# Optimization experiments

Measured on AMD Instinct MI355X. Metric: run time of the kernel, lower is better.

The kernel has to match this reference:

```python
import jax, jax.numpy as jnp
import numpy as np

B, S, D, H = 4, 2048, 512, 8
HD = D // H  # head width = 64

def setup_inputs() -> dict:
    key = jax.random.key(0)
    ks = jax.random.split(key, 7)
    x = jax.random.normal(ks[0], (B, S, D), dtype=jnp.float32)
    mask = jnp.ones((B, S), dtype=jnp.int32)
    # torch nn.Linear(dim, dim): weight [out, in], bias [out]
    sc = 1.0 / np.sqrt(D)
    Wq = jax.random.uniform(ks[1], (D, D), jnp.float32, -sc, sc)
    bq = jax.random.uniform(ks[2], (D,), jnp.float32, -sc, sc)
    Wk = jax.random.uniform(ks[3], (D, D), jnp.float32, -sc, sc)
    bk = jax.random.uniform(ks[4], (D,), jnp.float32, -sc, sc)
    Wv = jax.random.uniform(ks[5], (D, D), jnp.float32, -sc, sc)
    bv = jax.random.uniform(ks[6], (D,), jnp.float32, -sc, sc)
    return {"x": x, "mask": mask, "Wq": Wq, "bq": bq, "Wk": Wk, "bk": bk, "Wv": Wv, "bv": bv}

def reference(x, mask, Wq, bq, Wk, bk, Wv, bv):
    # QKV projections (torch Linear: x @ W.T + b)
    q = jnp.einsum('bsd,ed->bse', x, Wq) + bq
    k = jnp.einsum('bsd,ed->bse', x, Wk) + bk
    v = jnp.einsum('bsd,ed->bse', x, Wv) + bv
    # split heads -> (B, H, S, HD)
    q = q.reshape(B, S, H, HD).transpose(0, 2, 1, 3)
    k = k.reshape(B, S, H, HD).transpose(0, 2, 1, 3)
    v = v.reshape(B, S, H, HD).transpose(0, 2, 1, 3)
    scores = jnp.einsum('bhqd,bhkd->bhqk', q, k) / np.sqrt(HD).astype(np.float32)
    m = mask[:, None, None, :].astype(scores.dtype)  # (B,1,1,S)
    scores = scores - 10000.0 * (1.0 - m)
    attn = jax.nn.softmax(scores, axis=-1)  # dropout is identity in eval mode
    h = jnp.einsum('bhqk,bhkd->bhqd', attn, v)
    h = h.transpose(0, 2, 1, 3).reshape(B, S, D)
    return h
```

## Files before the change

### kernel.cpp

```cpp
#include <hip/hip_runtime.h>
#include <hip/hip_bf16.h>

#define Bb 4
#define Ss 2048
#define Dd 512
#define Hh 8
#define HD 64
#define NX (Bb*Ss*Dd)
#define NW (3*Dd*Dd)

typedef __attribute__((ext_vector_type(8))) short bf8_t;
typedef __attribute__((ext_vector_type(4))) float f4_t;
typedef unsigned int u32;
typedef __attribute__((ext_vector_type(4))) unsigned int u32x4;

typedef const unsigned int __attribute__((address_space(1)))* gas_t;
typedef unsigned int __attribute__((address_space(3)))* las_t;

#define LOG2E 1.44269504088896f
#define MBIAS_C (-10000.0f * LOG2E)

template<bool V> struct BoolC { static constexpr bool value = V; };

__device__ __forceinline__ short cvt1(float f) {
  __hip_bfloat16 h = __float2bfloat16(f);
  union { __hip_bfloat16 hh; short ss; } u; u.hh = h; return u.ss;
}

__device__ __forceinline__ u32 pkrn(float a, float b) {
  union { __hip_bfloat162 h2; u32 u; } v;
  v.h2 = __float22bfloat162_rn(make_float2(a, b));
  return v.u;
}

__device__ __forceinline__ bf8_t pack8(float4 f0, float4 f1) {
  union { bf8_t v8; u32x4 u4; } u;
  u.u4.x = pkrn(f0.x, f0.y); u.u4.y = pkrn(f0.z, f0.w);
  u.u4.z = pkrn(f1.x, f1.y); u.u4.w = pkrn(f1.z, f1.w);
  return u.v8;
}

__device__ __forceinline__ void gload_lds16(const void* g, void* l) {
  __builtin_amdgcn_global_load_lds((gas_t)g, (las_t)l, 16, 0, 0);
}

__global__ __launch_bounds__(256) void convert_kernel(
    const float* __restrict__ x, const float* __restrict__ Wq,
    const float* __restrict__ Wk, const float* __restrict__ Wv,
    short* __restrict__ xb, short* __restrict__ Wb)
{
  size_t i = ((size_t)blockIdx.x * 256 + threadIdx.x) * 8;
  const float* src; short* dst;
  if (i < (size_t)NX) { src = x + i; dst = xb + i; }
  else {
    size_t j = i - NX;
    int ws = (int)(j >> 18);
    const float* W = (ws == 0) ? Wq : (ws == 1) ? Wk : Wv;
    src = W + (j & 0x3FFFF); dst = Wb + j;
  }
  float4 f0 = *(const float4*)src;
  float4 f1 = *(const float4*)(src + 4);
  *(bf8_t*)dst = pack8(f0, f1);
}

__global__ __launch_bounds__(256, 2) void qkv_proj_kernel(
    const short* __restrict__ xb, const short* __restrict__ Wb,
    const float* __restrict__ bq, const float* __restrict__ bk,
    const float* __restrict__ bv,
    short* __restrict__ Qg, short* __restrict__ Kg, short* __restrict__ Vtg)
{
  __shared__ short SM[32768];
  short* As0 = SM;
  short* Bs0 = SM + 16384;
  const int p = blockIdx.y >> 2;
  const short* __restrict__ W = Wb + (size_t)p * Dd * Dd;
  const float* __restrict__ bias = (p==0) ? bq : (p==1) ? bk : bv;
  const int m0 = blockIdx.x * 128;
  const int n0 = (blockIdx.y & 3) * 128;
  const int tid = threadIdx.x;
  const int lane = tid & 63, wid = tid >> 6;
  const int lq = lane & 15, hi = lane >> 4;
  const int wm = wid & 1, wn = wid >> 1;

  const short* aSrc[4];
  const short* bSrc[4];
  #pragma unroll
  for (int i = 0; i < 4; i++) {
    int slot = tid + i*256, row = slot >> 3, c = slot & 7;
    aSrc[i] = xb + (size_t)(m0 + row)*Dd + ((c ^ (row&7))*8);
    bSrc[i] = W  + (size_t)(n0 + row)*Dd + ((c ^ (row&7))*8);
  }

  int aoff[2][4], boff[2][4];
  #pragma unroll
  for (int ks = 0; ks < 2; ks++) {
    const int cu = ks*4 + hi;
    #pragma unroll
    for (int mi = 0; mi < 4; mi++) {
      int row = wm*64 + mi*16 + lq;
      aoff[ks][mi] = (row*64 + ((cu ^ (row&7))*8)) * 2;
    }
    #pragma unroll
    for (int nf = 0; nf < 4; nf++) {
      int row = wn*64 + nf*16 + lq;
      boff[ks][nf] = (row*64 + ((cu ^ (row&7))*8)) * 2;
    }
  }

  const f4_t zero4 = {0.f, 0.f, 0.f, 0.f};
  f4_t acc[4][4];
  #pragma unroll
  for (int i = 0; i < 4; i++)
    #pragma unroll
    for (int j = 0; j < 4; j++) acc[i][j] = zero4;

  auto STAGE = [&](int bufi, int k0) {
    #pragma unroll
    for (int i = 0; i < 4; i++) {
      gload_lds16(aSrc[i] + k0, As0 + bufi*8192 + (tid + i*256)*8);
      gload_lds16(bSrc[i] + k0, Bs0 + bufi*8192 + (tid + i*256)*8);
    }
  };

  STAGE(0, 0);
  __syncthreads();
  #pragma unroll 2
  for (int kt = 0; kt < 8; kt++) {
    const int cur = kt & 1;
    if (kt < 7) STAGE(cur ^ 1, (kt + 1)*64);
    const char* ab = (const char*)(As0 + cur*8192);
    const char* bbp = (const char*)(Bs0 + cur*8192);
    #pragma unroll
    for (int ks = 0; ks < 2; ks++) {
      bf8_t a[4], bfrag[4];
      #pragma unroll
      for (int mi = 0; mi < 4; mi++) a[mi] = *(const bf8_t*)(ab + aoff[ks][mi]);
      #pragma unroll
      for (int nf = 0; nf < 4; nf++) bfrag[nf] = *(const bf8_t*)(bbp + boff[ks][nf]);
      #pragma unroll
      for (int mi = 0; mi < 4; mi++)
        #pragma unroll
        for (int nf = 0; nf < 4; nf++)
          acc[mi][nf] = __builtin_amdgcn_mfma_f32_16x16x32_bf16(a[mi], bfrag[nf], acc[mi][nf], 0, 0, 0);
    }
    __syncthreads();
  }

  const float qs = (p == 0) ? 0.125f * LOG2E : 1.0f;
  float badd[4];
  #pragma unroll
  for (int nf = 0; nf < 4; nf++) badd[nf] = bias[n0 + wn*64 + nf*16 + lq];

  if (p == 2) {
    short* VL = SM;
    #pragma unroll
    for (int mi = 0; mi < 4; mi++)
      #pragma unroll
      for (int nf = 0; nf < 4; nf++) {
        const int colh = wn*64 + nf*16 + lq;
        #pragma unroll
        for (int r = 0; r < 4; r++) {
          int rowm = wm*64 + mi*16 + hi*4 + r;
          VL[colh*136 + rowm] = cvt1(acc[mi][nf][r] + badd[nf]);
        }
      }
    __syncthreads();
    const int row = tid >> 1, half = tid & 1;
    const int colg = n0 + row, hh = colg >> 6, hd = colg & 63;
    const int bb = m0 >> 11, ssb = (m0 & 2047) + half*64;
    short* dst = Vtg + (((size_t)bb*Hh + hh)*HD + hd)*Ss + ssb;
    const short* src = VL + row*136 + half*64;
    #pragma unroll
    for (int j = 0; j < 8; j++)
      *(bf8_t*)(dst + j*8) = *(const bf8_t*)(src + j*8);
  } else {
    #pragma unroll
    for (int mi = 0; mi < 4; mi++) {
      #pragma unroll
      for (int nf = 0; nf < 4; nf++) {
        const int col = n0 + wn*64 + nf*16 + lq;
        const int h = col >> 6, hd = col & 63;
        #pragma unroll
        for (int r = 0; r < 4; r++) {
          int mrow = m0 + wm*64 + mi*16 + hi*4 + r;
          int bb = mrow >> 11, ss = mrow & (Ss-1);
          short val = cvt1((acc[mi][nf][r] + badd[nf]) * qs);
          if (p == 0)
            Qg[(((size_t)bb*Hh + h)*Ss + ss)*HD + hd] = val;
          else
            Kg[(((size_t)bb*Hh + h)*Ss + ss)*HD + hd] = val;
        }
      }
    }
  }
}

__global__ __launch_bounds__(256, 2) void attn_kernel(
    const short* __restrict__ Qg, const short* __restrict__ Kg,
    const short* __restrict__ Vtg, const int* __restrict__ mask,
    float* __restrict__ out)
{
  __shared__ short Ks[2][128*64];
  __shared__ short Vs[2][2][64*64];
  const int bh = blockIdx.x;
  const int b = bh >> 3, h = bh & 7;
  const int tid = threadIdx.x, lane = tid & 63, w = tid >> 6;
  const int hi = lane >> 4, lq = lane & 15;
  const short* __restrict__ Qb = Qg + (size_t)bh * Ss * HD;
  const short* __restrict__ Kb = Kg + (size_t)bh * Ss * HD;
  const short* __restrict__ Vb = Vtg + (size_t)bh * HD * Ss;
  const int* __restrict__ maskb = mask + b * Ss;
  const int q0 = blockIdx.y * 128 + w * 32;
  const int NT = Ss / 128;

  u32 mvbits = 0;
  #pragma unroll
  for (int t = 0; t < 32; t++)
    mvbits |= (maskb[t*64 + lane] != 0 ? 1u : 0u) << t;

  bf8_t qf[2][2];
  #pragma unroll
  for (int qg = 0; qg < 2; qg++)
    #pragma unroll
    for (int ks = 0; ks < 2; ks++)
      qf[qg][ks] = *(const bf8_t*)(Qb + (size_t)(q0 + qg*16 + lq)*HD + ks*32 + hi*8);

  int koffs[4][2], voffs[4][2];
  #pragma unroll
  for (int kb = 0; kb < 4; kb++) {
    int row = kb*16 + lq;
    #pragma unroll
    for (int ks = 0; ks < 2; ks++)
      koffs[kb][ks] = (row*64 + ((ks*4 + hi) ^ (row&7))*8) * 2;
  }
  #pragma unroll
  for (int nf2 = 0; nf2 < 4; nf2++) {
    int vr = nf2*16 + lq;
    #pragma unroll
    for (int ks2 = 0; ks2 < 2; ks2++)
      voffs[nf2][ks2] = (vr*64 + ((ks2*4 + hi) ^ (vr&7))*8) * 2;
  }

  const f4_t zero4 = {0.f, 0.f, 0.f, 0.f};
  f4_t o0[4], o1[4];
  #pragma unroll
  for (int j = 0; j < 4; j++) { o0[j] = zero4; o1[j] = zero4; }
  f4_t lacc0 = zero4, lacc1 = zero4;

  const bf8_t ones = {(short)0x3F80,(short)0x3F80,(short)0x3F80,(short)0x3F80,
                      (short)0x3F80,(short)0x3F80,(short)0x3F80,(short)0x3F80};

  const short* ksrcS[4];
  const short* vsrcS[4];
  int kslot[4], vslot[4];
  #pragma unroll
  for (int i = 0; i < 4; i++) {
    int s = tid + i*256;
    kslot[i] = s;
    int krow = s >> 3, kc = s & 7;
    ksrcS[i] = Kb + (size_t)krow*HD + ((kc ^ (krow&7))*8);
    vslot[i] = s;
    int vrow = (s >> 3) & 63, vc = s & 7;
    vsrcS[i] = Vb + (size_t)vrow*Ss + ((vc ^ (vrow&7))*8) + (s >> 9)*64;
  }

  auto STAGE = [&](int bufi, int kv) {
    #pragma unroll
    for (int i = 0; i < 4; i++)
      gload_lds16(ksrcS[i] + (size_t)kv*HD, &Ks[bufi][kslot[i]*8]);
    #pragma unroll
    for (int i = 0; i < 4; i++)
      gload_lds16(vsrcS[i] + kv, &Vs[bufi][0][vslot[i]*8]);
  };

  auto PASS = [&](auto maskedTag, int t, int p, const char* kbase, const char* vbase) {
    constexpr bool MASKED = decltype(maskedTag)::value;
    f4_t sa[4], sb[4];
    #pragma unroll
    for (int kb = 0; kb < 4; kb++) {
      bf8_t kf0 = *(const bf8_t*)(kbase + koffs[kb][0]);
      bf8_t kf1 = *(const bf8_t*)(kbase + koffs[kb][1]);
      sa[kb] = __builtin_amdgcn_mfma_f32_16x16x32_bf16(kf0, qf[0][0], zero4, 0, 0, 0);
      sa[kb] = __builtin_amdgcn_mfma_f32_16x16x32_bf16(kf1, qf[0][1], sa[kb], 0, 0, 0);
      sb[kb] = __builtin_amdgcn_mfma_f32_16x16x32_bf16(kf0, qf[1][0], zero4, 0, 0, 0);
      sb[kb] = __builtin_amdgcn_mfma_f32_16x16x32_bf16(kf1, qf[1][1], sb[kb], 0, 0, 0);
    }
    bf8_t vf[4][2];
    #pragma unroll
    for (int nf2 = 0; nf2 < 4; nf2++)
      #pragma unroll
      for (int ks2 = 0; ks2 < 2; ks2++)
        vf[nf2][ks2] = *(const bf8_t*)(vbase + voffs[nf2][ks2]);

    if (MASKED) {
      const bool mok = (mvbits >> (t*2 + p)) & 1u;
      if (__any(!mok)) {
        float mbl = mok ? 0.0f : MBIAS_C;
        #pragma unroll
        for (int kb = 0; kb < 4; kb++)
          #pragma unroll
          for (int r = 0; r < 4; r++) {
            float mm = __shfl(mbl, kb*16 + hi*4 + r, 64);
            sa[kb][r] += mm; sb[kb][r] += mm;
          }
      }
    }
    bf8_t pf0[2], pf1[2];
    {
      u32 Wa[4][2], Wbp[4][2];
      #pragma unroll
      for (int kb = 0; kb < 4; kb++) {
        Wa[kb][0] = pkrn(__builtin_amdgcn_exp2f(sa[kb][0]), __builtin_amdgcn_exp2f(sa[kb][1]));
        Wa[kb][1] = pkrn(__builtin_amdgcn_exp2f(sa[kb][2]), __builtin_amdgcn_exp2f(sa[kb][3]));
        Wbp[kb][0] = pkrn(__builtin_amdgcn_exp2f(sb[kb][0]), __builtin_amdgcn_exp2f(sb[kb][1]));
        Wbp[kb][1] = pkrn(__builtin_amdgcn_exp2f(sb[kb][2]), __builtin_amdgcn_exp2f(sb[kb][3]));
      }
      #pragma unroll
      for (int c = 0; c < 2; c++) {
        u32 ma[4], mb[4];
        #pragma unroll
        for (int d = 0; d < 2; d++) {
          u32 X = Wa[2*c][d], Y = Wa[2*c+1][d];
          asm volatile("v_permlane32_swap_b32 %0, %1" : "+v"(X), "+v"(Y));
          asm volatile("v_permlane16_swap_b32 %0, %1" : "+v"(X), "+v"(Y));
          ma[d]     = X;
          ma[2 + d] = Y;
          u32 X2 = Wbp[2*c][d], Y2 = Wbp[2*c+1][d];
          asm volatile("v_permlane32_swap_b32 %0, %1" : "+v"(X2), "+v"(Y2));
          asm volatile("v_permlane16_swap_b32 %0, %1" : "+v"(X2), "+v"(Y2));
          mb[d]     = X2;
          mb[2 + d] = Y2;
        }
        union { bf8_t v8; u32x4 u4; } pa, pb;
        pa.u4.x = ma[0]; pa.u4.y = ma[1]; pa.u4.z = ma[2]; pa.u4.w = ma[3];
        pb.u4.x = mb[0]; pb.u4.y = mb[1]; pb.u4.z = mb[2]; pb.u4.w = mb[3];
        pf0[c] = pa.v8; pf1[c] = pb.v8;
      }
    }
    __builtin_amdgcn_s_setprio(1);
    lacc0 = __builtin_amdgcn_mfma_f32_16x16x32_bf16(pf0[0], ones, lacc0, 0, 0, 0);
    lacc0 = __builtin_amdgcn_mfma_f32_16x16x32_bf16(pf0[1], ones, lacc0, 0, 0, 0);
    lacc1 = __builtin_amdgcn_mfma_f32_16x16x32_bf16(pf1[0], ones, lacc1, 0, 0, 0);
    lacc1 = __builtin_amdgcn_mfma_f32_16x16x32_bf16(pf1[1], ones, lacc1, 0, 0, 0);
    #pragma unroll
    for (int nf2 = 0; nf2 < 4; nf2++) {
      #pragma unroll
      for (int ks2 = 0; ks2 < 2; ks2++) {
        o0[nf2] = __builtin_amdgcn_mfma_f32_16x16x32_bf16(pf0[ks2], vf[nf2][ks2], o0[nf2], 0, 0, 0);
        o1[nf2] = __builtin_amdgcn_mfma_f32_16x16x32_bf16(pf1[ks2], vf[nf2][ks2], o1[nf2], 0, 0, 0);
      }
    }
    __builtin_amdgcn_s_setprio(0);
  };

  auto RUN = [&](auto maskedTag) {
    STAGE(0, 0);
    __syncthreads();
    #pragma unroll 2
    for (int t = 0; t < NT; t++) {
      const int cur = t & 1;
      if (t + 1 < NT) STAGE(cur ^ 1, (t + 1)*128);
      #pragma unroll
      for (int p = 0; p < 2; p++)
        PASS(maskedTag, t, p, (const char*)&Ks[cur][0] + p*8192,
             (const char*)&Vs[cur][p][0]);
      __syncthreads();
    }
  };

  const bool anymasked = __any(mvbits != 0xFFFFFFFFu);
  if (anymasked) RUN(BoolC<true>{});
  else           RUN(BoolC<false>{});

  #pragma unroll
  for (int nf2 = 0; nf2 < 4; nf2++)
    #pragma unroll
    for (int r = 0; r < 4; r++) {
      int srow0 = q0 + hi*4 + r;
      int srow1 = q0 + 16 + hi*4 + r;
      out[((size_t)(b*Ss + srow0))*Dd + h*HD + nf2*16 + lq] = o0[nf2][r] / lacc0[r];
      out[((size_t)(b*Ss + srow1))*Dd + h*HD + nf2*16 + lq] = o1[nf2][r] / lacc1[r];
    }
}

extern "C" void kernel_launch(void* const* d_in, const int* in_sizes, int n_in,
                              void* d_out, int out_size, void* d_ws, size_t ws_size,
                              hipStream_t stream) {
  const float* x  = (const float*)d_in[0];
  const int* mask = (const int*)d_in[1];
  const float* Wq = (const float*)d_in[2];
  const float* bq = (const float*)d_in[3];
  const float* Wk = (const float*)d_in[4];
  const float* bk = (const float*)d_in[5];
  const float* Wv = (const float*)d_in[6];
  const float* bv = (const float*)d_in[7];
  float* out = (float*)d_out;

  short* Qg = (short*)d_ws;
  short* Kg = Qg + (size_t)Bb*Hh*Ss*HD;
  short* Vt = Kg + (size_t)Bb*Hh*Ss*HD;
  short* xb = Vt + (size_t)Bb*Hh*Ss*HD;
  short* Wb = xb + (size_t)NX;

  convert_kernel<<<dim3((NX + NW)/2048), 256, 0, stream>>>(x, Wq, Wk, Wv, xb, Wb);
  qkv_proj_kernel<<<dim3(64, 12), 256, 0, stream>>>(xb, Wb, bq, bk, bv, Qg, Kg, Vt);
  attn_kernel<<<dim3(32, 16), 256, 0, stream>>>(Qg, Kg, Vt, mask, out);
}
```

Before: 77.30 us.

## Use two waves per attention block with 64 query rows per wave

The attention kernel now launches 128 threads per block instead of 256, and each wave handles 64 query rows (four 16-row groups) instead of 32. Each K/V fragment read from LDS is reused across twice as many query rows, which halves LDS read traffic per unit of MFMA work. In exchange each wave holds more accumulator and Q registers, each thread issues twice as many global-to-LDS loads per tile, and there are half as many waves per block to hide latency. Launch bounds change to (128,1), giving the compiler more register room.

Result: slower. 84.88 us (+9.8%).

```diff
diff --git a/kernel.cpp b/kernel.cpp
--- a/kernel.cpp
+++ b/kernel.cpp
@@ -195,7 +195,7 @@
   }
 }
 
-__global__ __launch_bounds__(256, 2) void attn_kernel(
+__global__ __launch_bounds__(128, 1) void attn_kernel(
     const short* __restrict__ Qg, const short* __restrict__ Kg,
     const short* __restrict__ Vtg, const int* __restrict__ mask,
     float* __restrict__ out)
@@ -210,7 +210,7 @@
   const short* __restrict__ Kb = Kg + (size_t)bh * Ss * HD;
   const short* __restrict__ Vb = Vtg + (size_t)bh * HD * Ss;
   const int* __restrict__ maskb = mask + b * Ss;
-  const int q0 = blockIdx.y * 128 + w * 32;
+  const int q0 = blockIdx.y * 128 + w * 64;
   const int NT = Ss / 128;
 
   u32 mvbits = 0;
@@ -218,9 +218,9 @@
   for (int t = 0; t < 32; t++)
     mvbits |= (maskb[t*64 + lane] != 0 ? 1u : 0u) << t;
 
-  bf8_t qf[2][2];
-  #pragma unroll
-  for (int qg = 0; qg < 2; qg++)
+  bf8_t qf[4][2];
+  #pragma unroll
+  for (int qg = 0; qg < 4; qg++)
     #pragma unroll
     for (int ks = 0; ks < 2; ks++)
       qf[qg][ks] = *(const bf8_t*)(Qb + (size_t)(q0 + qg*16 + lq)*HD + ks*32 + hi*8);
@@ -242,48 +242,47 @@
   }
 
   const f4_t zero4 = {0.f, 0.f, 0.f, 0.f};
-  f4_t o0[4], o1[4];
-  #pragma unroll
-  for (int j = 0; j < 4; j++) { o0[j] = zero4; o1[j] = zero4; }
-  f4_t lacc0 = zero4, lacc1 = zero4;
+  f4_t o[4][4];
+  #pragma unroll
+  for (int qg = 0; qg < 4; qg++)
+    #pragma unroll
+    for (int j = 0; j < 4; j++) o[qg][j] = zero4;
+  f4_t la[4];
+  #pragma unroll
+  for (int qg = 0; qg < 4; qg++) la[qg] = zero4;
 
   const bf8_t ones = {(short)0x3F80,(short)0x3F80,(short)0x3F80,(short)0x3F80,
                       (short)0x3F80,(short)0x3F80,(short)0x3F80,(short)0x3F80};
 
-  const short* ksrcS[4];
-  const short* vsrcS[4];
-  int kslot[4], vslot[4];
-  #pragma unroll
-  for (int i = 0; i < 4; i++) {
-    int s = tid + i*256;
-    kslot[i] = s;
+  const short* ksrcS[8];
+  const short* vsrcS[8];
+  int kvslot[8];
+  #pragma unroll
+  for (int i = 0; i < 8; i++) {
+    int s = tid + i*128;
+    kvslot[i] = s;
     int krow = s >> 3, kc = s & 7;
     ksrcS[i] = Kb + (size_t)krow*HD + ((kc ^ (krow&7))*8);
-    vslot[i] = s;
     int vrow = (s >> 3) & 63, vc = s & 7;
     vsrcS[i] = Vb + (size_t)vrow*Ss + ((vc ^ (vrow&7))*8) + (s >> 9)*64;
   }
 
   auto STAGE = [&](int bufi, int kv) {
     #pragma unroll
-    for (int i = 0; i < 4; i++)
-      gload_lds16(ksrcS[i] + (size_t)kv*HD, &Ks[bufi][kslot[i]*8]);
-    #pragma unroll
-    for (int i = 0; i < 4; i++)
-      gload_lds16(vsrcS[i] + kv, &Vs[bufi][0][vslot[i]*8]);
+    for (int i = 0; i < 8; i++)
+      gload_lds16(ksrcS[i] + (size_t)kv*HD, &Ks[bufi][kvslot[i]*8]);
+    #pragma unroll
+    for (int i = 0; i < 8; i++)
+      gload_lds16(vsrcS[i] + kv, &Vs[bufi][0][kvslot[i]*8]);
   };
 
   auto PASS = [&](auto maskedTag, int t, int p, const char* kbase, const char* vbase) {
     constexpr bool MASKED = decltype(maskedTag)::value;
-    f4_t sa[4], sb[4];
+    bf8_t kf[4][2];
     #pragma unroll
     for (int kb = 0; kb < 4; kb++) {
-      bf8_t kf0 = *(const bf8_t*)(kbase + koffs[kb][0]);
-      bf8_t kf1 = *(const bf8_t*)(kbase + koffs[kb][1]);
-      sa[kb] = __builtin_amdgcn_mfma_f32_16x16x32_bf16(kf0, qf[0][0], zero4, 0, 0, 0);
-      sa[kb] = __builtin_amdgcn_mfma_f32_16x16x32_bf16(kf1, qf[0][1], sa[kb], 0, 0, 0);
-      sb[kb] = __builtin_amdgcn_mfma_f32_16x16x32_bf16(kf0, qf[1][0], zero4, 0, 0, 0);
-      sb[kb] = __builtin_amdgcn_mfma_f32_16x16x32_bf16(kf1, qf[1][1], sb[kb], 0, 0, 0);
+      kf[kb][0] = *(const bf8_t*)(kbase + koffs[kb][0]);
+      kf[kb][1] = *(const bf8_t*)(kbase + koffs[kb][1]);
     }
     bf8_t vf[4][2];
     #pragma unroll
@@ -292,65 +291,82 @@
       for (int ks2 = 0; ks2 < 2; ks2++)
         vf[nf2][ks2] = *(const bf8_t*)(vbase + voffs[nf2][ks2]);
 
+    float mbl = 0.0f;
+    bool domask = false;
     if (MASKED) {
       const bool mok = (mvbits >> (t*2 + p)) & 1u;
-      if (__any(!mok)) {
-        float mbl = mok ? 0.0f : MBIAS_C;
-        #pragma unroll
-        for (int kb = 0; kb < 4; kb++)
+      domask = __any(!mok);
+      mbl = mok ? 0.0f : MBIAS_C;
+    }
+
+    #pragma unroll
+    for (int pr = 0; pr < 2; pr++) {
+      f4_t sa[4], sb[4];
+      #pragma unroll
+      for (int kb = 0; kb < 4; kb++) {
+        sa[kb] = __builtin_amdgcn_mfma_f32_16x16x32_bf16(kf[kb][0], qf[2*pr][0], zero4, 0, 0, 0);
+        sa[kb] = __builtin_amdgcn_mfma_f32_16x16x32_bf16(kf[kb][1], qf[2*pr][1], sa[kb], 0, 0, 0);
+        sb[kb] = __builtin_amdgcn_mfma_f32_16x16x32_bf16(kf[kb][0], qf[2*pr+1][0], zero4, 0, 0, 0);
+        sb[kb] = __builtin_amdgcn_mfma_f32_16x16x32_bf16(kf[kb][1], qf[2*pr+1][1], sb[kb], 0, 0, 0);
+      }
+      if (MASKED) {
+        if (domask) {
           #pragma unroll
-          for (int r = 0; r < 4; r++) {
-            float mm = __shfl(mbl, kb*16 + hi*4 + r, 64);
-            sa[kb][r] += mm; sb[kb][r] += mm;
+          for (int kb = 0; kb < 4; kb++)
+            #pragma unroll
+            for (int r = 0; r < 4; r++) {
+              float mm = __shfl(mbl, kb*16 + hi*4 + r, 64);
+              sa[kb][r] += mm; sb[kb][r] += mm;
+            }
+        }
+      }
+      bf8_t pf0[2], pf1[2];
+      {
+        u32 Wa[4][2], Wbp[4][2];
+        #pragma unroll
+        for (int kb = 0; kb < 4; kb++) {
+          Wa[kb][0] = pkrn(__builtin_amdgcn_exp2f(sa[kb][0]), __builtin_amdgcn_exp2f(sa[kb][1]));
+          Wa[kb][1] = pkrn(__builtin_amdgcn_exp2f(sa[kb][2]), __builtin_amdgcn_exp2f(sa[kb][3]));
+          Wbp[kb][0] = pkrn(__builtin_amdgcn_exp2f(sb[kb][0]), __builtin_amdgcn_exp2f(sb[kb][1]));
+          Wbp[kb][1] = pkrn(__builtin_amdgcn_exp2f(sb[kb][2]), __builtin_amdgcn_exp2f(sb[kb][3]));
+        }
+        #pragma unroll
+        for (int c = 0; c < 2; c++) {
+          u32 ma[4], mb[4];
+          #pragma unroll
+          for (int d = 0; d < 2; d++) {
+            u32 X = Wa[2*c][d], Y = Wa[2*c+1][d];
+            asm volatile("v_permlane32_swap_b32 %0, %1" : "+v"(X), "+v"(Y));
+            asm volatile("v_permlane16_swap_b32 %0, %1" : "+v"(X), "+v"(Y));
+            ma[d]     = X;
+            ma[2 + d] = Y;
+            u32 X2 = Wbp[2*c][d], Y2 = Wbp[2*c+1][d];
+            asm volatile("v_permlane32_swap_b32 %0, %1" : "+v"(X2), "+v"(Y2));
+            asm volatile("v_permlane16_swap_b32 %0, %1" : "+v"(X2), "+v"(Y2));
+            mb[d]     = X2;
+            mb[2 + d] = Y2;
           }
-      }
-    }
-    bf8_t pf0[2], pf1[2];
-    {
-      u32 Wa[4][2], Wbp[4][2];
-      #pragma unroll
-      for (int kb = 0; kb < 4; kb++) {
-        Wa[kb][0] = pkrn(__builtin_amdgcn_exp2f(sa[kb][0]), __builtin_amdgcn_exp2f(sa[kb][1]));
-        Wa[kb][1] = pkrn(__builtin_amdgcn_exp2f(sa[kb][2]), __builtin_amdgcn_exp2f(sa[kb][3]));
-        Wbp[kb][0] = pkrn(__builtin_amdgcn_exp2f(sb[kb][0]), __builtin_amdgcn_exp2f(sb[kb][1]));
-        Wbp[kb][1] = pkrn(__builtin_amdgcn_exp2f(sb[kb][2]), __builtin_amdgcn_exp2f(sb[kb][3]));
-      }
-      #pragma unroll
-      for (int c = 0; c < 2; c++) {
-        u32 ma[4], mb[4];
-        #pragma unroll
-        for (int d = 0; d < 2; d++) {
-          u32 X = Wa[2*c][d], Y = Wa[2*c+1][d];
-          asm volatile("v_permlane32_swap_b32 %0, %1" : "+v"(X), "+v"(Y));
-          asm volatile("v_permlane16_swap_b32 %0, %1" : "+v"(X), "+v"(Y));
-          ma[d]     = X;
-          ma[2 + d] = Y;
-          u32 X2 = Wbp[2*c][d], Y2 = Wbp[2*c+1][d];
-          asm volatile("v_permlane32_swap_b32 %0, %1" : "+v"(X2), "+v"(Y2));
-          asm volatile("v_permlane16_swap_b32 %0, %1" : "+v"(X2), "+v"(Y2));
-          mb[d]     = X2;
-          mb[2 + d] = Y2;
-        }
-        union { bf8_t v8; u32x4 u4; } pa, pb;
-        pa.u4.x = ma[0]; pa.u4.y = ma[1]; pa.u4.z = ma[2]; pa.u4.w = ma[3];
-        pb.u4.x = mb[0]; pb.u4.y = mb[1]; pb.u4.z = mb[2]; pb.u4.w = mb[3];
-        pf0[c] = pa.v8; pf1[c] = pb.v8;
-      }
-    }
-    __builtin_amdgcn_s_setprio(1);
-    lacc0 = __builtin_amdgcn_mfma_f32_16x16x32_bf16(pf0[0], ones, lacc0, 0, 0, 0);
-    lacc0 = __builtin_amdgcn_mfma_f32_16x16x32_bf16(pf0[1], ones, lacc0, 0, 0, 0);
-    lacc1 = __builtin_amdgcn_mfma_f32_16x16x32_bf16(pf1[0], ones, lacc1, 0, 0, 0);
-    lacc1 = __builtin_amdgcn_mfma_f32_16x16x32_bf16(pf1[1], ones, lacc1, 0, 0, 0);
-    #pragma unroll
-    for (int nf2 = 0; nf2 < 4; nf2++) {
-      #pragma unroll
-      for (int ks2 = 0; ks2 < 2; ks2++) {
-        o0[nf2] = __builtin_amdgcn_mfma_f32_16x16x32_bf16(pf0[ks2], vf[nf2][ks2], o0[nf2], 0, 0, 0);
-        o1[nf2] = __builtin_amdgcn_mfma_f32_16x16x32_bf16(pf1[ks2], vf[nf2][ks2], o1[nf2], 0, 0, 0);
-      }
-    }
-    __builtin_amdgcn_s_setprio(0);
+          union { bf8_t v8; u32x4 u4; } pa, pb;
+          pa.u4.x = ma[0]; pa.u4.y = ma[1]; pa.u4.z = ma[2]; pa.u4.w = ma[3];
+          pb.u4.x = mb[0]; pb.u4.y = mb[1]; pb.u4.z = mb[2]; pb.u4.w = mb[3];
+          pf0[c] = pa.v8; pf1[c] = pb.v8;
+        }
+      }
+      __builtin_amdgcn_s_setprio(1);
+      la[2*pr]   = __builtin_amdgcn_mfma_f32_16x16x32_bf16(pf0[0], ones, la[2*pr], 0, 0, 0);
+      la[2*pr]   = __builtin_amdgcn_mfma_f32_16x16x32_bf16(pf0[1], ones, la[2*pr], 0, 0, 0);
+      la[2*pr+1] = __builtin_amdgcn_mfma_f32_16x16x32_bf16(pf1[0], ones, la[2*pr+1], 0, 0, 0);
+      la[2*pr+1] = __builtin_amdgcn_mfma_f32_16x16x32_bf16(pf1[1], ones, la[2*pr+1], 0, 0, 0);
+      #pragma unroll
+      for (int nf2 = 0; nf2 < 4; nf2++) {
+        #pragma unroll
+        for (int ks2 = 0; ks2 < 2; ks2++) {
+          o[2*pr][nf2]   = __builtin_amdgcn_mfma_f32_16x16x32_bf16(pf0[ks2], vf[nf2][ks2], o[2*pr][nf2], 0, 0, 0);
+          o[2*pr+1][nf2] = __builtin_amdgcn_mfma_f32_16x16x32_bf16(pf1[ks2], vf[nf2][ks2], o[2*pr+1][nf2], 0, 0, 0);
+        }
+      }
+      __builtin_amdgcn_s_setprio(0);
+    }
   };
 
   auto RUN = [&](auto maskedTag) {
@@ -373,14 +389,14 @@
   else           RUN(BoolC<false>{});
 
   #pragma unroll
-  for (int nf2 = 0; nf2 < 4; nf2++)
-    #pragma unroll
-    for (int r = 0; r < 4; r++) {
-      int srow0 = q0 + hi*4 + r;
-      int srow1 = q0 + 16 + hi*4 + r;
-      out[((size_t)(b*Ss + srow0))*Dd + h*HD + nf2*16 + lq] = o0[nf2][r] / lacc0[r];
-      out[((size_t)(b*Ss + srow1))*Dd + h*HD + nf2*16 + lq] = o1[nf2][r] / lacc1[r];
-    }
+  for (int qg = 0; qg < 4; qg++)
+    #pragma unroll
+    for (int nf2 = 0; nf2 < 4; nf2++)
+      #pragma unroll
+      for (int r = 0; r < 4; r++) {
+        int srow = q0 + qg*16 + hi*4 + r;
+        out[((size_t)(b*Ss + srow))*Dd + h*HD + nf2*16 + lq] = o[qg][nf2][r] / la[qg][r];
+      }
 }
 
 extern "C" void kernel_launch(void* const* d_in, const int* in_sizes, int n_in,
@@ -404,5 +420,5 @@
 
   convert_kernel<<<dim3((NX + NW)/2048), 256, 0, stream>>>(x, Wq, Wk, Wv, xb, Wb);
   qkv_proj_kernel<<<dim3(64, 12), 256, 0, stream>>>(xb, Wb, bq, bk, bv, Qg, Kg, Vt);
-  attn_kernel<<<dim3(32, 16), 256, 0, stream>>>(Qg, Kg, Vt, mask, out);
-}
+  attn_kernel<<<dim3(32, 16), 128, 0, stream>>>(Qg, Kg, Vt, mask, out);
+}
```
